# Kernel tuning notes

Measured on AMD Instinct MI355X. Metric: run time of the kernel, lower is better.

The kernel has to match this reference:

```python
import jax, jax.numpy as jnp
import numpy as np

B, N, Y, C = 8, 512, 64, 256


def setup_inputs() -> dict:
    key = jax.random.key(0)
    ks = jax.random.split(key, 7)
    sampled = jax.random.normal(ks[0], (B, N, Y, C), dtype=jnp.float32)
    # binary visibility mask (original passes 0/1-ish validity)
    valid = jnp.round(jax.random.uniform(ks[1], (B, N, Y), dtype=jnp.float32))
    # buffer: normalized y depth steps, y_steps = arange(Y)
    y_steps = jnp.arange(Y, dtype=jnp.float32)
    y_norm = (y_steps - y_steps.min()) / jnp.maximum(y_steps.max() - y_steps.min(), 1e-6)
    # weight_mlp = Linear(C+1 -> C), GELU, Linear(C -> 1); store weights pre-transposed (in, out)
    s1 = 1.0 / np.sqrt(C + 1)
    s2 = 1.0 / np.sqrt(C)
    W1 = jax.random.uniform(ks[2], (C + 1, C), dtype=jnp.float32, minval=-s1, maxval=s1)
    b1 = jax.random.uniform(ks[3], (C,), dtype=jnp.float32, minval=-s1, maxval=s1)
    W2 = jax.random.uniform(ks[4], (C, 1), dtype=jnp.float32, minval=-s2, maxval=s2)
    b2 = jax.random.uniform(ks[5], (1,), dtype=jnp.float32, minval=-s2, maxval=s2)
    return {"sampled": sampled, "valid": valid, "y_norm": y_norm,
            "W1": W1, "b1": b1, "W2": W2, "b2": b2}


def reference(sampled, valid, y_norm, W1, b1, W2, b2):
    b, n, y, c = sampled.shape
    yfeat = jnp.broadcast_to(y_norm.reshape(1, 1, y, 1), (b, n, y, 1))
    feat = jnp.concatenate([sampled, yfeat], axis=-1)            # [B,N,Y,C+1]
    h = jax.nn.gelu(feat @ W1 + b1, approximate=False)            # [B,N,Y,C]
    logits = (h @ W2 + b2)[..., 0]                                # [B,N,Y]
    logits = jnp.where(valid < 0.5, jnp.float32(-10000.0), logits)
    weights = jax.nn.softmax(logits, axis=-1) * valid
    denom = jnp.maximum(weights.sum(axis=-1, keepdims=True), 1e-6)
    weights = weights / denom
    return jnp.einsum('bnyc,bny->bnc', sampled, weights)          # [B,N,C]
```

## Files before the change

### kernel.cpp

```cpp
#include <hip/hip_runtime.h>

#define NTOK 4096
#define AST  264

using short8  = __attribute__((ext_vector_type(8))) short;
using short4v = __attribute__((ext_vector_type(4))) short;
using floatx4 = __attribute__((ext_vector_type(4))) float;

static __device__ __forceinline__ short f2bf(float f) {
  union { float f; unsigned u; } v; v.f = f;
  unsigned u = v.u;
  u = (u + 0x7fffu + ((u >> 16) & 1u)) >> 16;
  return (short)u;
}

__global__ void prep_w1(const float* __restrict__ W1, short* __restrict__ W1s) {
  int T = blockIdx.x * 256 + threadIdx.x;
  int j = T & 7;
  int l = (T >> 3) & 63;
  int t = (T >> 9) & 15;
  int s = T >> 13;
  int k = s * 32 + (l >> 4) * 8 + j;
  int n = t * 16 + (l & 15);
  W1s[T] = f2bf(W1[k * 256 + n]);
}

__global__ void __launch_bounds__(256) agg_kernel(
    const float* __restrict__ sampled, const float* __restrict__ valid,
    const float* __restrict__ y_norm, const float* __restrict__ W1,
    const float* __restrict__ b1, const float* __restrict__ W2,
    const float* __restrict__ b2, const short* __restrict__ W1s,
    float* __restrict__ out) {
  __shared__ __align__(16) short Abf[64 * AST];
  __shared__ float wlog[4][64];
  __shared__ float wts[64];
  __shared__ float ynl[64];

  const int tid = threadIdx.x;
  const int tok = blockIdx.x;
  const float* S = sampled + ((size_t)tok << 14);

  if (tid < 64) ynl[tid] = y_norm[tid];
  #pragma unroll
  for (int it = 0; it < 16; ++it) {
    int j  = it * 256 + tid;
    int y  = j >> 6;
    int k4 = (j & 63) << 2;
    float4 v = ((const float4*)S)[j];
    short4v p;
    p[0] = f2bf(v.x); p[1] = f2bf(v.y); p[2] = f2bf(v.z); p[3] = f2bf(v.w);
    *(short4v*)(&Abf[y * AST + k4]) = p;
  }
  __syncthreads();

  const int wv  = tid >> 6;
  const int ln  = tid & 63;
  const int q   = ln >> 4;
  const int c15 = ln & 15;

  const floatx4 fzero = {0.f, 0.f, 0.f, 0.f};
  floatx4 acc[4][4];
  #pragma unroll
  for (int mt = 0; mt < 4; ++mt)
    #pragma unroll
    for (int nt = 0; nt < 4; ++nt) acc[mt][nt] = fzero;

  #pragma unroll
  for (int s = 0; s < 8; ++s) {
    short8 af[4];
    #pragma unroll
    for (int mt = 0; mt < 4; ++mt)
      af[mt] = *(const short8*)(&Abf[(mt * 16 + c15) * AST + s * 32 + q * 8]);
    #pragma unroll
    for (int nt = 0; nt < 4; ++nt) {
      const int t = wv * 4 + nt;
      short8 bfrag = *(const short8*)(W1s + (((s * 16 + t) * 64 + ln) << 3));
      #pragma unroll
      for (int mt = 0; mt < 4; ++mt)
        acc[mt][nt] = __builtin_amdgcn_mfma_f32_16x16x32_bf16(af[mt], bfrag, acc[mt][nt], 0, 0, 0);
    }
  }

  float w2v[4], b1v[4], wlv[4];
  #pragma unroll
  for (int nt = 0; nt < 4; ++nt) {
    int n = wv * 64 + nt * 16 + c15;
    w2v[nt] = W2[n];
    b1v[nt] = b1[n];
    wlv[nt] = W1[65536 + n];
  }
  #pragma unroll
  for (int mt = 0; mt < 4; ++mt) {
    #pragma unroll
    for (int r = 0; r < 4; ++r) {
      int m = mt * 16 + q * 4 + r;
      float ym = ynl[m];
      float p = 0.f;
      #pragma unroll
      for (int nt = 0; nt < 4; ++nt) {
        float z = acc[mt][nt][r] + ym * wlv[nt] + b1v[nt];
        float h = 0.5f * z * (1.0f + erff(z * 0.70710678118654752f));
        p += h * w2v[nt];
      }
      p += __shfl_xor(p, 1);
      p += __shfl_xor(p, 2);
      p += __shfl_xor(p, 4);
      p += __shfl_xor(p, 8);
      if (c15 == 0) wlog[wv][m] = p;
    }
  }
  __syncthreads();

  if (tid < 64) {
    float lg = wlog[0][tid] + wlog[1][tid] + wlog[2][tid] + wlog[3][tid] + b2[0];
    float v  = valid[tok * 64 + tid];
    float lm = (v < 0.5f) ? -10000.0f : lg;
    float mx = lm;
    #pragma unroll
    for (int d = 32; d > 0; d >>= 1) mx = fmaxf(mx, __shfl_xor(mx, d));
    float e  = expf(lm - mx);
    float s1 = e;
    #pragma unroll
    for (int d = 32; d > 0; d >>= 1) s1 += __shfl_xor(s1, d);
    float wgt = e / s1 * v;
    float s2  = wgt;
    #pragma unroll
    for (int d = 32; d > 0; d >>= 1) s2 += __shfl_xor(s2, d);
    wts[tid] = wgt / fmaxf(s2, 1e-6f);
  }
  __syncthreads();

  float a0 = 0.f;
  #pragma unroll 8
  for (int y = 0; y < 64; ++y)
    a0 = fmaf(S[(y << 8) + tid], wts[y], a0);
  out[(size_t)tok * 256 + tid] = a0;
}

extern "C" void kernel_launch(void* const* d_in, const int* in_sizes, int n_in,
                              void* d_out, int out_size, void* d_ws, size_t ws_size,
                              hipStream_t stream) {
  const float* sampled = (const float*)d_in[0];
  const float* valid   = (const float*)d_in[1];
  const float* y_norm  = (const float*)d_in[2];
  const float* W1      = (const float*)d_in[3];
  const float* b1      = (const float*)d_in[4];
  const float* W2      = (const float*)d_in[5];
  const float* b2      = (const float*)d_in[6];
  short* W1s = (short*)d_ws;
  float* out = (float*)d_out;

  prep_w1<<<256, 256, 0, stream>>>(W1, W1s);
  agg_kernel<<<NTOK, 256, 0, stream>>>(sampled, valid, y_norm, W1, b1, W2, b2, W1s, out);
}
```

Before: 452.4 us.

## Reuse bf16 tile for weighted sum, fast GELU, batched loads, redundant softmax

The final weighted sum now reads the bf16 copy of the samples already in shared memory instead of re-reading fp32 from global memory. Exact erf-based GELU becomes an Abramowitz-Stegun polynomial using the hardware reciprocal and fast exp. The global-to-LDS load issues 8 float4 loads before converting, and every wave computes the softmax redundantly so one barrier goes away. Also adds launch bounds for 4 blocks per CU and a vectorized weight-prep kernel. This saves a second global pass over the input, but the output now uses bf16-rounded samples and an approximate GELU, so accuracy drops.

```diff
diff --git a/kernel.cpp b/kernel.cpp
--- a/kernel.cpp
+++ b/kernel.cpp
@@ -14,18 +14,38 @@
   return (short)u;
 }
 
-__global__ void prep_w1(const float* __restrict__ W1, short* __restrict__ W1s) {
-  int T = blockIdx.x * 256 + threadIdx.x;
-  int j = T & 7;
-  int l = (T >> 3) & 63;
-  int t = (T >> 9) & 15;
-  int s = T >> 13;
-  int k = s * 32 + (l >> 4) * 8 + j;
-  int n = t * 16 + (l & 15);
-  W1s[T] = f2bf(W1[k * 256 + n]);
+static __device__ __forceinline__ float bf2f(short s) {
+  union { unsigned u; float f; } v; v.u = ((unsigned)(unsigned short)s) << 16;
+  return v.f;
 }
 
-__global__ void __launch_bounds__(256) agg_kernel(
+static __device__ __forceinline__ float fast_gelu(float z) {
+  float x  = z * 0.70710678118654752f;
+  float ax = fabsf(x);
+  float t  = __builtin_amdgcn_rcpf(fmaf(0.3275911f, ax, 1.0f));
+  float em = __expf(-ax * ax);
+  float p  = fmaf(fmaf(fmaf(fmaf(1.061405429f, t, -1.453152027f), t,
+                            1.421413741f), t, -0.284496736f), t, 0.254829592f);
+  float er = fmaf(-p * t, em, 1.0f);
+  unsigned sgn = __float_as_uint(x) & 0x80000000u;
+  er = __uint_as_float(__float_as_uint(er) | sgn);
+  return z * fmaf(0.5f, er, 0.5f);
+}
+
+__global__ void prep_w1(const float* __restrict__ W1, short* __restrict__ W1s) {
+  const int n  = threadIdx.x;
+  const int kb = blockIdx.x;
+  const int s  = kb >> 2;
+  const int l  = ((kb & 3) << 4) | (n & 15);
+  const int t  = n >> 4;
+  short8 o;
+  #pragma unroll
+  for (int j = 0; j < 8; ++j)
+    o[j] = f2bf(W1[(kb * 8 + j) * 256 + n]);
+  *(short8*)(W1s + (((s * 16 + t) * 64 + l) << 3)) = o;
+}
+
+__global__ void __launch_bounds__(256, 4) agg_kernel(
     const float* __restrict__ sampled, const float* __restrict__ valid,
     const float* __restrict__ y_norm, const float* __restrict__ W1,
     const float* __restrict__ b1, const float* __restrict__ W2,
@@ -33,7 +53,6 @@
     float* __restrict__ out) {
   __shared__ __align__(16) short Abf[64 * AST];
   __shared__ float wlog[4][64];
-  __shared__ float wts[64];
   __shared__ float ynl[64];
 
   const int tid = threadIdx.x;
@@ -41,15 +60,22 @@
   const float* S = sampled + ((size_t)tok << 14);
 
   if (tid < 64) ynl[tid] = y_norm[tid];
+  const float4* S4 = (const float4*)S;
   #pragma unroll
-  for (int it = 0; it < 16; ++it) {
-    int j  = it * 256 + tid;
-    int y  = j >> 6;
-    int k4 = (j & 63) << 2;
-    float4 v = ((const float4*)S)[j];
-    short4v p;
-    p[0] = f2bf(v.x); p[1] = f2bf(v.y); p[2] = f2bf(v.z); p[3] = f2bf(v.w);
-    *(short4v*)(&Abf[y * AST + k4]) = p;
+  for (int h = 0; h < 2; ++h) {
+    float4 v[8];
+    #pragma unroll
+    for (int it = 0; it < 8; ++it) v[it] = S4[(h * 8 + it) * 256 + tid];
+    #pragma unroll
+    for (int it = 0; it < 8; ++it) {
+      int j  = (h * 8 + it) * 256 + tid;
+      int y  = j >> 6;
+      int k4 = (j & 63) << 2;
+      short4v p;
+      p[0] = f2bf(v[it].x); p[1] = f2bf(v[it].y);
+      p[2] = f2bf(v[it].z); p[3] = f2bf(v[it].w);
+      *(short4v*)(&Abf[y * AST + k4]) = p;
+    }
   }
   __syncthreads();
 
@@ -99,8 +125,7 @@
       #pragma unroll
       for (int nt = 0; nt < 4; ++nt) {
         float z = acc[mt][nt][r] + ym * wlv[nt] + b1v[nt];
-        float h = 0.5f * z * (1.0f + erff(z * 0.70710678118654752f));
-        p += h * w2v[nt];
+        p += fast_gelu(z) * w2v[nt];
       }
       p += __shfl_xor(p, 1);
       p += __shfl_xor(p, 2);
@@ -111,29 +136,28 @@
   }
   __syncthreads();
 
-  if (tid < 64) {
-    float lg = wlog[0][tid] + wlog[1][tid] + wlog[2][tid] + wlog[3][tid] + b2[0];
-    float v  = valid[tok * 64 + tid];
-    float lm = (v < 0.5f) ? -10000.0f : lg;
-    float mx = lm;
-    #pragma unroll
-    for (int d = 32; d > 0; d >>= 1) mx = fmaxf(mx, __shfl_xor(mx, d));
-    float e  = expf(lm - mx);
-    float s1 = e;
-    #pragma unroll
-    for (int d = 32; d > 0; d >>= 1) s1 += __shfl_xor(s1, d);
-    float wgt = e / s1 * v;
-    float s2  = wgt;
-    #pragma unroll
-    for (int d = 32; d > 0; d >>= 1) s2 += __shfl_xor(s2, d);
-    wts[tid] = wgt / fmaxf(s2, 1e-6f);
-  }
-  __syncthreads();
+  float lg = wlog[0][ln] + wlog[1][ln] + wlog[2][ln] + wlog[3][ln] + b2[0];
+  float vv = valid[tok * 64 + ln];
+  float lm = (vv < 0.5f) ? -10000.0f : lg;
+  float mx = lm;
+  #pragma unroll
+  for (int d = 32; d > 0; d >>= 1) mx = fmaxf(mx, __shfl_xor(mx, d));
+  float e  = __expf(lm - mx);
+  float s1 = e;
+  #pragma unroll
+  for (int d = 32; d > 0; d >>= 1) s1 += __shfl_xor(s1, d);
+  float wgt = e / s1 * vv;
+  float s2  = wgt;
+  #pragma unroll
+  for (int d = 32; d > 0; d >>= 1) s2 += __shfl_xor(s2, d);
+  wgt = wgt / fmaxf(s2, 1e-6f);
 
   float a0 = 0.f;
-  #pragma unroll 8
-  for (int y = 0; y < 64; ++y)
-    a0 = fmaf(S[(y << 8) + tid], wts[y], a0);
+  #pragma unroll
+  for (int y = 0; y < 64; ++y) {
+    float wy = __shfl(wgt, y);
+    a0 = fmaf(bf2f(Abf[y * AST + tid]), wy, a0);
+  }
   out[(size_t)tok * 256 + tid] = a0;
 }
 
@@ -150,6 +174,6 @@
   short* W1s = (short*)d_ws;
   float* out = (float*)d_out;
 
-  prep_w1<<<256, 256, 0, stream>>>(W1, W1s);
+  prep_w1<<<32, 256, 0, stream>>>(W1, W1s);
   agg_kernel<<<NTOK, 256, 0, stream>>>(sampled, valid, y_norm, W1, b1, W2, b2, W1s, out);
 }
```

Measured after the change: 411.5 us. -9.0%, faster.
